# Performance work log

Measured on AMD Instinct MI355X. Metric: run time of the kernel, lower is better.

## Reference

```python
import jax, jax.numpy as jnp
import numpy as np

D_MODEL = 1024
NUM_HEADS = 16
HEAD_DIM = D_MODEL // NUM_HEADS


def setup_inputs() -> dict:
    key = jax.random.key(0)
    ks = jax.random.split(key, 9)
    s = 1.0 / np.sqrt(D_MODEL)
    def lin(k):
        kw, kb = jax.random.split(k)
        W = jax.random.uniform(kw, (D_MODEL, D_MODEL), jnp.float32, -s, s)
        b = jax.random.uniform(kb, (D_MODEL,), jnp.float32, -s, s)
        return W, b
    Wq, bq = lin(ks[0])
    Wk, bk = lin(ks[1])
    Wv, bv = lin(ks[2])
    Wo, bo = lin(ks[3])
    x = jax.random.normal(ks[4], (4, 2048, D_MODEL), jnp.float32)
    return {"x": x, "Wq": Wq, "bq": bq, "Wk": Wk, "bk": bk,
            "Wv": Wv, "bv": bv, "Wo": Wo, "bo": bo}


def reference(x, Wq, bq, Wk, bk, Wv, bv, Wo, bo):
    B, S, _ = x.shape
    def heads(W, b):
        # [B,S,D] -> [B,H,S,Dh]
        return (x @ W.T + b).reshape(B, S, NUM_HEADS, HEAD_DIM).transpose(0, 2, 1, 3)
    q = heads(Wq, bq)
    k = heads(Wk, bk)
    v = heads(Wv, bv)
    scale = jnp.sqrt(jnp.float32(HEAD_DIM))
    scores = jnp.einsum('bhqd,bhkd->bhqk', q, k) / scale  # [B,H,S,S]
    attn = jax.nn.softmax(scores, axis=-1)
    ctx = jnp.einsum('bhqk,bhkd->bhqd', attn, v)
    ctx = ctx.transpose(0, 2, 1, 3).reshape(B, S, D_MODEL)
    out = ctx @ Wo.T + bo
    return out
```

## Files before the change

### kernel.cpp

```cpp
#include <hip/hip_runtime.h>
#include <hip/hip_bf16.h>

typedef __bf16 bf16;
typedef __attribute__((ext_vector_type(2))) __bf16 bf16x2;
typedef __attribute__((ext_vector_type(4))) __bf16 bf16x4;
typedef __attribute__((ext_vector_type(8))) __bf16 bf16x8;
typedef __attribute__((ext_vector_type(4))) float floatx4;

#define MFMA_16x16x32(a, b, c) __builtin_amdgcn_mfma_f32_16x16x32_bf16((a), (b), (c), 0, 0, 0)

#define SOFTMAX_SC 0.18033688011112042f

__device__ __forceinline__ void async_lds16(const bf16* g, bf16* lds) {
  __builtin_amdgcn_global_load_lds(
      (__attribute__((address_space(1))) void*)(g),
      (__attribute__((address_space(3))) void*)(lds),
      16, 0, 0);
}

__global__ __launch_bounds__(256) void cast_all_kernel(
    const float* __restrict__ x,
    const float* __restrict__ Wq, const float* __restrict__ Wk,
    const float* __restrict__ Wv, const float* __restrict__ Wo,
    bf16* __restrict__ dst)
{
  const size_t xN = (size_t)8192 * 1024;
  size_t i = ((size_t)blockIdx.x * 256 + threadIdx.x) * 8;
  const float* src;
  size_t off;
  if (i < xN) { src = x; off = i; }
  else {
    size_t j = i - xN;
    int w = (int)(j >> 20);
    off = j & (((size_t)1 << 20) - 1);
    src = (w == 0) ? Wq : (w == 1) ? Wk : (w == 2) ? Wv : Wo;
  }
  floatx4 a = *(const floatx4*)(src + off);
  floatx4 b = *(const floatx4*)(src + off + 4);
  bf16x8 r;
  r[0] = (bf16)a[0]; r[1] = (bf16)a[1]; r[2] = (bf16)a[2]; r[3] = (bf16)a[3];
  r[4] = (bf16)b[0]; r[5] = (bf16)b[1]; r[6] = (bf16)b[2]; r[7] = (bf16)b[3];
  *(bf16x8*)(dst + i) = r;
}

template <typename CT>
__device__ __forceinline__ void gemm128_async_body(
    const bf16* __restrict__ A, const bf16* __restrict__ W,
    const float* __restrict__ bias, CT* __restrict__ C,
    int gm0, int gn0)
{
  __shared__ __align__(16) bf16 As[128 * 64];
  __shared__ __align__(16) bf16 Bs[128 * 64];

  const int tid  = threadIdx.x;
  const int lane = tid & 63;
  const int wave = tid >> 6;
  const int quad = lane >> 4;
  const int l15  = lane & 15;

  const int m_off = (wave >> 1) * 64;
  const int n_off = (wave & 1) * 64;

  floatx4 acc[4][4] = {};

  const bf16* ap[4];
  const bf16* wp[4];
  #pragma unroll
  for (int i = 0; i < 4; ++i) {
    int c = i * 256 + tid;
    int srow = c >> 3;
    int ksw  = (c & 7) ^ (srow & 7);
    ap[i] = A + (size_t)(gm0 + srow) * 1024 + ksw * 8;
    wp[i] = W + (size_t)(gn0 + srow) * 1024 + ksw * 8;
  }

  for (int kt = 0; kt < 16; ++kt) {
    __syncthreads();
    #pragma unroll
    for (int i = 0; i < 4; ++i) {
      int c = i * 256 + tid;
      async_lds16(ap[i], &As[c * 8]);
      async_lds16(wp[i], &Bs[c * 8]);
      ap[i] += 64; wp[i] += 64;
    }
    __syncthreads();

    #pragma unroll
    for (int kk = 0; kk < 2; ++kk) {
      bf16x8 af[4], bfr[4];
      #pragma unroll
      for (int i = 0; i < 4; ++i) {
        int rm = m_off + i * 16 + l15;
        af[i]  = *(const bf16x8*)&As[rm * 64 + (((kk * 4 + quad) ^ (rm & 7)) * 8)];
        int rn = n_off + i * 16 + l15;
        bfr[i] = *(const bf16x8*)&Bs[rn * 64 + (((kk * 4 + quad) ^ (rn & 7)) * 8)];
      }
      #pragma unroll
      for (int i = 0; i < 4; ++i)
        #pragma unroll
        for (int j = 0; j < 4; ++j)
          acc[i][j] = MFMA_16x16x32(af[i], bfr[j], acc[i][j]);
    }
  }

  #pragma unroll
  for (int j = 0; j < 4; ++j) {
    const int gcol = gn0 + n_off + j * 16 + l15;
    const float bv = bias[gcol];
    #pragma unroll
    for (int i = 0; i < 4; ++i) {
      const int gr = gm0 + m_off + i * 16 + quad * 4;
      #pragma unroll
      for (int r = 0; r < 4; ++r)
        C[(size_t)(gr + r) * 1024 + gcol] = (CT)(acc[i][j][r] + bv);
    }
  }
}

__global__ __launch_bounds__(256) void o_gemm_async(
    const bf16* __restrict__ ctx, const bf16* __restrict__ Wob,
    const float* __restrict__ bo, float* __restrict__ out)
{
  const int flat = blockIdx.y * 8 + blockIdx.x;
  const int L = (flat & 7) * 64 + (flat >> 3);
  gemm128_async_body<float>(ctx, Wob, bo, out, (L >> 3) * 128, (L & 7) * 128);
}

__global__ __launch_bounds__(256) void qkv_gemm128(
    const bf16* __restrict__ xb,
    const bf16* __restrict__ Wqb, const float* __restrict__ bq,
    const bf16* __restrict__ Wkb, const float* __restrict__ bk,
    const bf16* __restrict__ Wvb, const float* __restrict__ bv,
    bf16* Q, bf16* K, bf16* Vt)
{
  __shared__ __align__(16) bf16 As[128 * 64];
  __shared__ __align__(16) bf16 Bs[128 * 64];

  const int flat = blockIdx.x + 8 * (blockIdx.y + 64 * blockIdx.z);
  const int L = (flat & 7) * 192 + (flat >> 3);
  const int z   = L >> 9;
  const int rem = L & 511;
  const int gy  = rem >> 3;
  const int gx  = rem & 7;

  const bf16* W = (z == 0) ? Wqb : (z == 1) ? Wkb : Wvb;
  const float* bias = (z == 0) ? bq : (z == 1) ? bk : bv;

  const int tid  = threadIdx.x;
  const int lane = tid & 63;
  const int wave = tid >> 6;
  const int quad = lane >> 4;
  const int l15  = lane & 15;

  const int gm0   = gy * 128;
  const int gn0   = gx * 128;
  const int m_off = (wave >> 1) * 64;
  const int n_off = (wave & 1) * 64;

  floatx4 acc[4][4] = {};

  const bf16* ap[4];
  const bf16* wp[4];
  #pragma unroll
  for (int i = 0; i < 4; ++i) {
    int c = i * 256 + tid;
    int srow = c >> 3;
    int ksw  = (c & 7) ^ (srow & 7);
    ap[i] = xb + (size_t)(gm0 + srow) * 1024 + ksw * 8;
    wp[i] = W + (size_t)(gn0 + srow) * 1024 + ksw * 8;
  }

  for (int kt = 0; kt < 16; ++kt) {
    __syncthreads();
    #pragma unroll
    for (int i = 0; i < 4; ++i) {
      int c = i * 256 + tid;
      async_lds16(ap[i], &As[c * 8]);
      async_lds16(wp[i], &Bs[c * 8]);
      ap[i] += 64; wp[i] += 64;
    }
    __syncthreads();

    #pragma unroll
    for (int kk = 0; kk < 2; ++kk) {
      bf16x8 af[4], bfr[4];
      #pragma unroll
      for (int i = 0; i < 4; ++i) {
        int rm = m_off + i * 16 + l15;
        af[i]  = *(const bf16x8*)&As[rm * 64 + (((kk * 4 + quad) ^ (rm & 7)) * 8)];
        int rn = n_off + i * 16 + l15;
        bfr[i] = *(const bf16x8*)&Bs[rn * 64 + (((kk * 4 + quad) ^ (rn & 7)) * 8)];
      }
      #pragma unroll
      for (int i = 0; i < 4; ++i)
        #pragma unroll
        for (int j = 0; j < 4; ++j)
          acc[i][j] = MFMA_16x16x32(af[i], bfr[j], acc[i][j]);
    }
  }

  #pragma unroll
  for (int j = 0; j < 4; ++j) {
    const int gcol = gn0 + n_off + j * 16 + l15;
    const float bv = bias[gcol];
    #pragma unroll
    for (int i = 0; i < 4; ++i) {
      const int gr = gm0 + m_off + i * 16 + quad * 4;
      if (z == 2) {
        const int h  = gcol >> 6;
        const int dh = gcol & 63;
        const size_t base =
            (((size_t)(gr >> 11) * 16 + h) * 64 + dh) * 2048 + (gr & 2047);
        bf16x4 pk;
        #pragma unroll
        for (int r = 0; r < 4; ++r) pk[r] = (bf16)(acc[i][j][r] + bv);
        *(bf16x4*)&Vt[base] = pk;
      } else {
        bf16* dst = (z == 0) ? Q : K;
        const float sc = (z == 0) ? SOFTMAX_SC : 1.0f;
        #pragma unroll
        for (int r = 0; r < 4; ++r)
          dst[(size_t)(gr + r) * 1024 + gcol] = (bf16)((acc[i][j][r] + bv) * sc);
      }
    }
  }
}

__global__ __launch_bounds__(512, 4) void flash11_kernel(
    const bf16* __restrict__ Q, const bf16* __restrict__ Kg,
    const bf16* __restrict__ Vtg, bf16* __restrict__ ctx)
{
  __shared__ __align__(16) bf16 Ks[2][64 * 64];
  __shared__ __align__(16) bf16 Vts[2][64 * 64];
  __shared__ __align__(16) bf16 Ps[8 * 32 * 72];

  const int tid  = threadIdx.x;
  const int lane = tid & 63;
  const int wave = tid >> 6;
  const int quad = lane >> 4;
  const int l15  = lane & 15;

  const int flat = blockIdx.y * 8 + blockIdx.x;
  const int L = (flat & 7) * 64 + (flat >> 3);
  const int qt = L & 7;
  const int bh = L >> 3;
  const int b  = bh >> 4;
  const int h  = bh & 15;

  const size_t row0 = (size_t)b * 2048;
  const int col0 = h * 64;

  const int qbase = qt * 256 + wave * 32;
  bf16x8 qf[2][2];
  #pragma unroll
  for (int q = 0; q < 2; ++q) {
    const bf16* qp = Q + (row0 + qbase + q * 16 + l15) * 1024 + col0 + quad * 8;
    qf[q][0] = *(const bf16x8*)(qp);
    qf[q][1] = *(const bf16x8*)(qp + 32);
  }

  floatx4 o_acc[2][4] = {};
  floatx4 l_acc[2] = {};

  bf16x8 onesf;
  #pragma unroll
  for (int i = 0; i < 8; ++i) onesf[i] = (bf16)1.0f;

  const int srow = tid >> 3;
  const int cell = (tid & 7) ^ (srow & 7);
  const bf16* kp = Kg + (row0 + srow) * 1024 + col0 + cell * 8;
  const bf16* vp = Vtg + ((size_t)bh * 64 + srow) * 2048 + cell * 8;
  const int soff = tid * 8;

  async_lds16(kp, &Ks[0][soff]);
  async_lds16(vp, &Vts[0][soff]);
  kp += 64 * 1024;
  vp += 64;

  int koffA[4], koffB[4], vOff[2][4];
  #pragma unroll
  for (int j = 0; j < 4; ++j) {
    const int rk = j * 16 + l15;
    koffA[j] = rk * 64 + ((quad ^ (rk & 7)) * 8);
    koffB[j] = rk * 64 + (((4 + quad) ^ (rk & 7)) * 8);
  }
  #pragma unroll
  for (int kk = 0; kk < 2; ++kk)
    #pragma unroll
    for (int t = 0; t < 4; ++t) {
      const int rd = t * 16 + l15;
      vOff[kk][t] = rd * 64 + (((kk * 4 + quad) ^ (rd & 7)) * 8);
    }
  const int pmask = l15 & 14;
  int pw_off[2][4];
  #pragma unroll
  for (int q = 0; q < 2; ++q)
    #pragma unroll
    for (int j = 0; j < 4; ++j)
      pw_off[q][j] = (wave * 32 + q * 16 + l15) * 72 + (((4 * j + quad) ^ pmask) * 4);
  int pr_off[2][2];
  #pragma unroll
  for (int q = 0; q < 2; ++q)
    #pragma unroll
    for (int kk = 0; kk < 2; ++kk)
      pr_off[q][kk] =
          (wave * 32 + q * 16 + l15) * 72 + (((8 * kk + 2 * quad) ^ pmask) * 4);

  for (int kb = 0; kb < 32; ++kb) {
    const int cur = kb & 1;
    const bf16* const Kc = Ks[cur];
    const bf16* const Vc = Vts[cur];

    __syncthreads();

    if (kb < 31) {
      async_lds16(kp, &Ks[cur ^ 1][soff]);
      async_lds16(vp, &Vts[cur ^ 1][soff]);
      kp += 64 * 1024;
      vp += 64;
    }

    #pragma unroll
    for (int j = 0; j < 4; ++j) {
      bf16x8 k0 = *(const bf16x8*)&Kc[koffA[j]];
      bf16x8 k1 = *(const bf16x8*)&Kc[koffB[j]];
      #pragma unroll
      for (int q = 0; q < 2; ++q) {
        floatx4 z = {};
        z = MFMA_16x16x32(k0, qf[q][0], z);
        z = MFMA_16x16x32(k1, qf[q][1], z);
        bf16x4 pk;
        #pragma unroll
        for (int r = 0; r < 4; ++r) pk[r] = (bf16)exp2f(z[r]);
        *(bf16x4*)&Ps[pw_off[q][j]] = pk;
      }
    }

    #pragma unroll
    for (int kk = 0; kk < 2; ++kk) {
      bf16x8 vf[4];
      #pragma unroll
      for (int t = 0; t < 4; ++t) vf[t] = *(const bf16x8*)&Vc[vOff[kk][t]];
      bf16x8 pf0 = *(const bf16x8*)&Ps[pr_off[0][kk]];
      bf16x8 pf1 = *(const bf16x8*)&Ps[pr_off[1][kk]];
      __builtin_amdgcn_s_setprio(1);
      #pragma unroll
      for (int t = 0; t < 4; ++t) {
        o_acc[0][t] = MFMA_16x16x32(pf0, vf[t], o_acc[0][t]);
        o_acc[1][t] = MFMA_16x16x32(pf1, vf[t], o_acc[1][t]);
      }
      l_acc[0] = MFMA_16x16x32(pf0, onesf, l_acc[0]);
      l_acc[1] = MFMA_16x16x32(pf1, onesf, l_acc[1]);
      __builtin_amdgcn_s_setprio(0);
    }
  }

  #pragma unroll
  for (int q = 0; q < 2; ++q) {
    floatx4 li;
    #pragma unroll
    for (int r = 0; r < 4; ++r) li[r] = 1.0f / l_acc[q][r];
    #pragma unroll
    for (int t = 0; t < 4; ++t) {
      const int gc = col0 + t * 16 + l15;
      #pragma unroll
      for (int r = 0; r < 4; ++r) {
        const int srow2 = qbase + q * 16 + quad * 4 + r;
        ctx[(row0 + srow2) * 1024 + gc] = (bf16)(o_acc[q][t][r] * li[r]);
      }
    }
  }
}

__device__ __forceinline__ bf16x8 load8(const bf16* p) { return *(const bf16x8*)p; }
__device__ __forceinline__ bf16x8 load8(const float* p) {
  floatx4 a = *(const floatx4*)p;
  floatx4 b = *(const floatx4*)(p + 4);
  bf16x8 r;
  r[0] = (bf16)a[0]; r[1] = (bf16)a[1]; r[2] = (bf16)a[2]; r[3] = (bf16)a[3];
  r[4] = (bf16)b[0]; r[5] = (bf16)b[1]; r[6] = (bf16)b[2]; r[7] = (bf16)b[3];
  return r;
}

template <typename AT, typename CT>
__device__ __forceinline__ void gemm128_body_fb(
    const AT* __restrict__ A, const float* __restrict__ W,
    const float* __restrict__ bias, CT* __restrict__ C)
{
  constexpr int LDP = 72;
  __shared__ __align__(16) bf16 As[128 * LDP];
  __shared__ __align__(16) bf16 Bs[128 * LDP];
  const int tid = threadIdx.x, lane = tid & 63, wave = tid >> 6;
  const int quad = lane >> 4, l15 = lane & 15;
  const int gm0 = blockIdx.y * 128, gn0 = blockIdx.x * 128;
  const int m_off = (wave >> 1) * 64, n_off = (wave & 1) * 64;
  floatx4 acc[4][4] = {};
  int srow[4], scol[4];
  #pragma unroll
  for (int i = 0; i < 4; ++i) {
    int c = i * 256 + tid;
    srow[i] = c >> 3; scol[i] = (c & 7) * 8;
  }
  for (int kt = 0; kt < 16; ++kt) {
    bf16x8 ar[4], br[4];
    #pragma unroll
    for (int i = 0; i < 4; ++i) {
      ar[i] = load8(A + (size_t)(gm0 + srow[i]) * 1024 + kt * 64 + scol[i]);
      br[i] = load8(W + (size_t)(gn0 + srow[i]) * 1024 + kt * 64 + scol[i]);
    }
    __syncthreads();
    #pragma unroll
    for (int i = 0; i < 4; ++i) {
      *(bf16x8*)&As[srow[i] * LDP + scol[i]] = ar[i];
      *(bf16x8*)&Bs[srow[i] * LDP + scol[i]] = br[i];
    }
    __syncthreads();
    #pragma unroll
    for (int kk = 0; kk < 2; ++kk) {
      bf16x8 af[4], bfr[4];
      #pragma unroll
      for (int i = 0; i < 4; ++i) {
        af[i]  = *(const bf16x8*)&As[(m_off + i * 16 + l15) * LDP + (kk * 4 + quad) * 8];
        bfr[i] = *(const bf16x8*)&Bs[(n_off + i * 16 + l15) * LDP + (kk * 4 + quad) * 8];
      }
      #pragma unroll
      for (int i = 0; i < 4; ++i)
        #pragma unroll
        for (int j = 0; j < 4; ++j)
          acc[i][j] = MFMA_16x16x32(af[i], bfr[j], acc[i][j]);
    }
  }
  #pragma unroll
  for (int j = 0; j < 4; ++j) {
    const int gcol = gn0 + n_off + j * 16 + l15;
    const float bv = bias[gcol];
    #pragma unroll
    for (int i = 0; i < 4; ++i) {
      const int gr = gm0 + m_off + i * 16 + quad * 4;
      #pragma unroll
      for (int r = 0; r < 4; ++r)
        C[(size_t)(gr + r) * 1024 + gcol] = (CT)(acc[i][j][r] + bv);
    }
  }
}

__global__ __launch_bounds__(256) void qkv_gemm_fb(
    const float* __restrict__ x,
    const float* __restrict__ Wq, const float* __restrict__ bq,
    const float* __restrict__ Wk, const float* __restrict__ bk,
    const float* __restrict__ Wv, const float* __restrict__ bv,
    bf16* Q, bf16* K, bf16* V)
{
  const float* W; const float* bias; bf16* out;
  if (blockIdx.z == 0)      { W = Wq; bias = bq; out = Q; }
  else if (blockIdx.z == 1) { W = Wk; bias = bk; out = K; }
  else                      { W = Wv; bias = bv; out = V; }
  gemm128_body_fb<float, bf16>(x, W, bias, out);
}

__global__ __launch_bounds__(256) void out_gemm_fb(
    const bf16* __restrict__ ctx, const float* __restrict__ Wo,
    const float* __restrict__ bo, float* __restrict__ out)
{
  gemm128_body_fb<bf16, float>(ctx, Wo, bo, out);
}

__global__ __launch_bounds__(512) void flash_fb(
    const bf16* Q, const bf16* __restrict__ Kg, const bf16* __restrict__ Vg,
    bf16* ctx)
{
  __shared__ __align__(16) bf16 Ks[64 * 72];
  __shared__ __align__(16) bf16 Vs[64 * 72];
  __shared__ __align__(16) bf16 Vt[64 * 72];
  __shared__ __align__(16) bf16 Ps[8 * 16 * 72];
  const int tid = threadIdx.x, lane = tid & 63, wave = tid >> 6;
  const int quad = lane >> 4, l15 = lane & 15;
  const int bh = blockIdx.y, b = bh >> 4, h = bh & 15, qt = blockIdx.x;
  const size_t row0 = (size_t)b * 2048;
  const int col0 = h * 64;
  const int qs = qt * 128 + wave * 16 + l15;
  const bf16* qp = Q + (row0 + qs) * 1024 + col0 + quad * 8;
  const bf16x8 qf0 = *(const bf16x8*)(qp);
  const bf16x8 qf1 = *(const bf16x8*)(qp + 32);
  floatx4 o_acc[4] = {};
  float l_part[4] = {0.0f, 0.0f, 0.0f, 0.0f};
  const float SC = SOFTMAX_SC;
  const int srow = tid >> 3, scol = (tid & 7) * 8;
  const bf16* kptr = Kg + (row0 + srow) * 1024 + col0 + scol;
  const bf16* vptr = Vg + (row0 + srow) * 1024 + col0 + scol;
  const int td = tid & 63, tg = tid >> 6;
  for (int kb = 0; kb < 32; ++kb) {
    bf16x8 kr = *(const bf16x8*)kptr;
    bf16x8 vr = *(const bf16x8*)vptr;
    kptr += 64 * 1024; vptr += 64 * 1024;
    __syncthreads();
    *(bf16x8*)&Ks[srow * 72 + scol] = kr;
    *(bf16x8*)&Vs[srow * 72 + scol] = vr;
    __syncthreads();
    {
      bf16x8 t;
      #pragma unroll
      for (int j = 0; j < 8; ++j) t[j] = Vs[(tg * 8 + j) * 72 + td];
      *(bf16x8*)&Vt[td * 72 + tg * 8] = t;
    }
    floatx4 sc[4];
    #pragma unroll
    for (int j = 0; j < 4; ++j) {
      int rk = j * 16 + l15;
      bf16x8 k0 = *(const bf16x8*)&Ks[rk * 72 + quad * 8];
      bf16x8 k1 = *(const bf16x8*)&Ks[rk * 72 + 32 + quad * 8];
      floatx4 z = {};
      z = MFMA_16x16x32(qf0, k0, z);
      z = MFMA_16x16x32(qf1, k1, z);
      sc[j] = z;
    }
    #pragma unroll
    for (int j = 0; j < 4; ++j)
      #pragma unroll
      for (int r = 0; r < 4; ++r) {
        float p = exp2f(fminf(sc[j][r] * SC, 60.0f));
        sc[j][r] = p;
        l_part[r] += p;
      }
    #pragma unroll
    for (int j = 0; j < 4; ++j)
      #pragma unroll
      for (int r = 0; r < 4; ++r)
        Ps[(wave * 16 + quad * 4 + r) * 72 + j * 16 + l15] = (bf16)sc[j][r];
    __syncthreads();
    #pragma unroll
    for (int kk = 0; kk < 2; ++kk) {
      bf16x8 pf = *(const bf16x8*)&Ps[(wave * 16 + l15) * 72 + kk * 32 + quad * 8];
      #pragma unroll
      for (int t = 0; t < 4; ++t) {
        bf16x8 vf = *(const bf16x8*)&Vt[(t * 16 + l15) * 72 + kk * 32 + quad * 8];
        o_acc[t] = MFMA_16x16x32(pf, vf, o_acc[t]);
      }
    }
  }
  #pragma unroll
  for (int off = 1; off < 16; off <<= 1)
    #pragma unroll
    for (int r = 0; r < 4; ++r)
      l_part[r] += __shfl_xor(l_part[r], off, 64);
  #pragma unroll
  for (int r = 0; r < 4; ++r) l_part[r] = 1.0f / l_part[r];
  #pragma unroll
  for (int t = 0; t < 4; ++t)
    #pragma unroll
    for (int r = 0; r < 4; ++r) {
      int srow2 = qt * 128 + wave * 16 + quad * 4 + r;
      ctx[(row0 + srow2) * 1024 + col0 + t * 16 + l15] = (bf16)(o_acc[t][r] * l_part[r]);
    }
}

extern "C" void kernel_launch(void* const* d_in, const int* in_sizes, int n_in,
                              void* d_out, int out_size, void* d_ws, size_t ws_size,
                              hipStream_t stream) {
  (void)in_sizes; (void)n_in; (void)out_size;
  const float* x  = (const float*)d_in[0];
  const float* Wq = (const float*)d_in[1];
  const float* bq = (const float*)d_in[2];
  const float* Wk = (const float*)d_in[3];
  const float* bk = (const float*)d_in[4];
  const float* Wv = (const float*)d_in[5];
  const float* bv = (const float*)d_in[6];
  const float* Wo = (const float*)d_in[7];
  const float* bo = (const float*)d_in[8];
  float* out = (float*)d_out;

  const size_t nE = (size_t)8192 * 1024;
  const size_t wE = (size_t)1024 * 1024;
  const size_t need = (5 * nE + 4 * wE) * sizeof(bf16);

  if (ws_size >= need) {
    bf16* Qw   = (bf16*)d_ws;
    bf16* Kw   = Qw + nE;
    bf16* Vtw  = Kw + nE;
    bf16* ctxw = Vtw + nE;
    bf16* xb   = ctxw + nE;
    bf16* Wqb  = xb + nE;
    bf16* Wkb  = Wqb + wE;
    bf16* Wvb  = Wkb + wE;
    bf16* Wob  = Wvb + wE;

    cast_all_kernel<<<dim3(6144), 256, 0, stream>>>(x, Wq, Wk, Wv, Wo, xb);

    qkv_gemm128<<<dim3(8, 64, 3), 256, 0, stream>>>(
        xb, Wqb, bq, Wkb, bk, Wvb, bv, Qw, Kw, Vtw);
    flash11_kernel<<<dim3(8, 64), 512, 0, stream>>>(Qw, Kw, Vtw, ctxw);
    o_gemm_async<<<dim3(8, 64), 256, 0, stream>>>(ctxw, Wob, bo, out);
  } else {
    bf16* Qw = (bf16*)d_ws;
    bf16* Kw = Qw + nE;
    bf16* Vw = Kw + nE;
    bf16* ctx = (ws_size >= 4 * nE * sizeof(bf16)) ? (Vw + nE) : Qw;
    qkv_gemm_fb<<<dim3(8, 64, 3), 256, 0, stream>>>(x, Wq, bq, Wk, bk, Wv, bv, Qw, Kw, Vw);
    flash_fb<<<dim3(16, 64), 512, 0, stream>>>(Qw, Kw, Vw, ctx);
    out_gemm_fb<<<dim3(8, 64), 256, 0, stream>>>(ctx, Wo, bo, out);
  }
}
```

Baseline: 281.8 us.

## Load K/V fragments directly from global memory instead of LDS double-buffering

The flash kernel drops the shared-memory double buffer for K and V tiles and the per-iteration block barrier. Each wave now reads its MFMA K and V fragments straight from global memory, relying on L2/L1 caching for the reuse across the 8 waves. The P staging buffer stride is shrunk from 72 to 64, and launch bounds are raised to 6 blocks per CU. This trades LDS traffic and barrier stalls for 8x redundant global/L2 reads of K/V and exposed load latency, and the P stride change may add bank conflicts.

```diff
diff --git a/kernel.cpp b/kernel.cpp
--- a/kernel.cpp
+++ b/kernel.cpp
@@ -226,13 +226,11 @@
   }
 }
 
-__global__ __launch_bounds__(512, 4) void flash11_kernel(
+__global__ __launch_bounds__(512, 6) void flash12_kernel(
     const bf16* __restrict__ Q, const bf16* __restrict__ Kg,
     const bf16* __restrict__ Vtg, bf16* __restrict__ ctx)
 {
-  __shared__ __align__(16) bf16 Ks[2][64 * 64];
-  __shared__ __align__(16) bf16 Vts[2][64 * 64];
-  __shared__ __align__(16) bf16 Ps[8 * 32 * 72];
+  __shared__ __align__(16) bf16 Ps[8 * 32 * 64];
 
   const int tid  = threadIdx.x;
   const int lane = tid & 63;
@@ -266,64 +264,32 @@
   #pragma unroll
   for (int i = 0; i < 8; ++i) onesf[i] = (bf16)1.0f;
 
-  const int srow = tid >> 3;
-  const int cell = (tid & 7) ^ (srow & 7);
-  const bf16* kp = Kg + (row0 + srow) * 1024 + col0 + cell * 8;
-  const bf16* vp = Vtg + ((size_t)bh * 64 + srow) * 2048 + cell * 8;
-  const int soff = tid * 8;
-
-  async_lds16(kp, &Ks[0][soff]);
-  async_lds16(vp, &Vts[0][soff]);
-  kp += 64 * 1024;
-  vp += 64;
-
-  int koffA[4], koffB[4], vOff[2][4];
-  #pragma unroll
-  for (int j = 0; j < 4; ++j) {
-    const int rk = j * 16 + l15;
-    koffA[j] = rk * 64 + ((quad ^ (rk & 7)) * 8);
-    koffB[j] = rk * 64 + (((4 + quad) ^ (rk & 7)) * 8);
-  }
-  #pragma unroll
-  for (int kk = 0; kk < 2; ++kk)
-    #pragma unroll
-    for (int t = 0; t < 4; ++t) {
-      const int rd = t * 16 + l15;
-      vOff[kk][t] = rd * 64 + (((kk * 4 + quad) ^ (rd & 7)) * 8);
-    }
+  const bf16* kgp = Kg + (row0 + l15) * 1024 + col0 + quad * 8;
+  const bf16* vgp = Vtg + ((size_t)bh * 64 + l15) * 2048 + quad * 8;
+
   const int pmask = l15 & 14;
   int pw_off[2][4];
   #pragma unroll
   for (int q = 0; q < 2; ++q)
     #pragma unroll
     for (int j = 0; j < 4; ++j)
-      pw_off[q][j] = (wave * 32 + q * 16 + l15) * 72 + (((4 * j + quad) ^ pmask) * 4);
+      pw_off[q][j] = (wave * 32 + q * 16 + l15) * 64 + (((4 * j + quad) ^ pmask) * 4);
   int pr_off[2][2];
   #pragma unroll
   for (int q = 0; q < 2; ++q)
     #pragma unroll
     for (int kk = 0; kk < 2; ++kk)
       pr_off[q][kk] =
-          (wave * 32 + q * 16 + l15) * 72 + (((8 * kk + 2 * quad) ^ pmask) * 4);
+          (wave * 32 + q * 16 + l15) * 64 + (((8 * kk + 2 * quad) ^ pmask) * 4);
 
   for (int kb = 0; kb < 32; ++kb) {
-    const int cur = kb & 1;
-    const bf16* const Kc = Ks[cur];
-    const bf16* const Vc = Vts[cur];
-
-    __syncthreads();
-
-    if (kb < 31) {
-      async_lds16(kp, &Ks[cur ^ 1][soff]);
-      async_lds16(vp, &Vts[cur ^ 1][soff]);
-      kp += 64 * 1024;
-      vp += 64;
-    }
+    const bf16* kc = kgp + (size_t)kb * 64 * 1024;
+    const bf16* vc = vgp + kb * 64;
 
     #pragma unroll
     for (int j = 0; j < 4; ++j) {
-      bf16x8 k0 = *(const bf16x8*)&Kc[koffA[j]];
-      bf16x8 k1 = *(const bf16x8*)&Kc[koffB[j]];
+      bf16x8 k0 = *(const bf16x8*)(kc + (size_t)j * 16 * 1024);
+      bf16x8 k1 = *(const bf16x8*)(kc + (size_t)j * 16 * 1024 + 32);
       #pragma unroll
       for (int q = 0; q < 2; ++q) {
         floatx4 z = {};
@@ -340,7 +306,8 @@
     for (int kk = 0; kk < 2; ++kk) {
       bf16x8 vf[4];
       #pragma unroll
-      for (int t = 0; t < 4; ++t) vf[t] = *(const bf16x8*)&Vc[vOff[kk][t]];
+      for (int t = 0; t < 4; ++t)
+        vf[t] = *(const bf16x8*)(vc + (size_t)t * 16 * 2048 + kk * 32);
       bf16x8 pf0 = *(const bf16x8*)&Ps[pr_off[0][kk]];
       bf16x8 pf1 = *(const bf16x8*)&Ps[pr_off[1][kk]];
       __builtin_amdgcn_s_setprio(1);
@@ -588,7 +555,7 @@
 
     qkv_gemm128<<<dim3(8, 64, 3), 256, 0, stream>>>(
         xb, Wqb, bq, Wkb, bk, Wvb, bv, Qw, Kw, Vtw);
-    flash11_kernel<<<dim3(8, 64), 512, 0, stream>>>(Qw, Kw, Vtw, ctxw);
+    flash12_kernel<<<dim3(8, 64), 512, 0, stream>>>(Qw, Kw, Vtw, ctxw);
     o_gemm_async<<<dim3(8, 64), 256, 0, stream>>>(ctxw, Wob, bo, out);
   } else {
     bf16* Qw = (bf16*)d_ws;
```

Result: slower. 566.7 us (+101.1%).
